# Performance work log

Hardware: AMD Instinct MI355X
Metric: run time of the kernel (lower is better)

Reference implementation:

```python
import jax, jax.numpy as jnp
import numpy as np

N_NODES = 100000
N_EDGES = 1000000
F_IN = 64
F_HID = 64
F_OUT = 2
NUM_GRAPHS = 64


def setup_inputs() -> dict:
    key = jax.random.key(0)
    ks = jax.random.split(key, 8)
    x = jax.random.normal(ks[0], (N_NODES, F_IN), dtype=jnp.float32)
    edge_index = jax.random.randint(ks[1], (2, N_EDGES), 0, N_NODES, dtype=jnp.int32)
    batch = jnp.sort(jax.random.randint(ks[2], (N_NODES,), 0, NUM_GRAPHS, dtype=jnp.int32))
    s1 = 1.0 / np.sqrt(F_IN)
    s2 = 1.0 / np.sqrt(F_HID)
    W1 = jax.random.normal(ks[3], (F_IN, F_HID), dtype=jnp.float32) * s1
    W2 = jax.random.normal(ks[4], (F_HID, F_HID), dtype=jnp.float32) * s2
    W3 = jax.random.normal(ks[5], (F_HID, F_HID), dtype=jnp.float32) * s2
    Wlin = jax.random.normal(ks[6], (F_HID, F_OUT), dtype=jnp.float32) * s2
    return {
        "x": x, "edge_index": edge_index, "batch": batch,
        "W1": W1, "b1": jnp.zeros((F_HID,), jnp.float32),
        "W2": W2, "b2": jnp.zeros((F_HID,), jnp.float32),
        "W3": W3, "b3": jnp.zeros((F_HID,), jnp.float32),
        "Wlin": Wlin, "blin": jnp.zeros((F_OUT,), jnp.float32),
    }


def _gcn_norm(edge_index, n_nodes):
    # add self-loops, compute symmetric D^-1/2 (A+I) D^-1/2 edge weights
    loops = jnp.arange(n_nodes, dtype=edge_index.dtype)
    src = jnp.concatenate([edge_index[0], loops])  # message source j
    dst = jnp.concatenate([edge_index[1], loops])  # aggregation target i
    deg = jax.ops.segment_sum(jnp.ones_like(dst, dtype=jnp.float32), dst,
                              num_segments=n_nodes)
    dinv = jnp.where(deg > 0, jax.lax.rsqrt(deg), 0.0)
    norm = dinv[src] * dinv[dst]  # [E+N]
    return src, dst, norm


def _gcn_conv(h, W, b, src, dst, norm, n_nodes):
    h = h @ W                                    # [N, F] dense transform first (PyG order)
    msg = h[src] * norm[:, None]                 # gather + scale  [E+N, F]
    agg = jax.ops.segment_sum(msg, dst, num_segments=n_nodes)
    return agg + b


def reference(x, edge_index, batch, W1, b1, W2, b2, W3, b3, Wlin, blin):
    n = x.shape[0]
    src, dst, norm = _gcn_norm(edge_index, n)
    h = jax.nn.relu(_gcn_conv(x, W1, b1, src, dst, norm, n))
    h = jax.nn.relu(_gcn_conv(h, W2, b2, src, dst, norm, n))
    h = _gcn_conv(h, W3, b3, src, dst, norm, n)
    # global mean pool over graphs
    sums = jax.ops.segment_sum(h, batch, num_segments=NUM_GRAPHS)        # [G, F]
    cnts = jax.ops.segment_sum(jnp.ones((n,), jnp.float32), batch,
                               num_segments=NUM_GRAPHS)
    pooled = sums / jnp.maximum(cnts, 1.0)[:, None]
    # dropout(p=0.1) is identity in eval mode
    return pooled @ Wlin + blin
```

## Files before the change

### kernel.cpp

```cpp
#include <hip/hip_runtime.h>

#define FDIM 64

typedef unsigned short u16;
typedef unsigned int u32;
typedef float v2f __attribute__((ext_vector_type(2)));

__device__ __forceinline__ u16 f2bf(float x) {
    unsigned int u = __float_as_uint(x);
    return (u16)((u + 0x7fff + ((u >> 16) & 1)) >> 16);
}
__device__ __forceinline__ float bf2f(u16 h) {
    return __uint_as_float(((unsigned int)h) << 16);
}
__device__ __forceinline__ u32 pk_fp8x4(float a, float b, float c, float d) {
    u32 p = __builtin_amdgcn_cvt_pk_fp8_f32(a, b, 0, false);
    p = __builtin_amdgcn_cvt_pk_fp8_f32(c, d, p, true);
    return p;
}


template <bool BF16IN>
__device__ __forceinline__ void mm_tile64(
    const void* __restrict__ ain, const float* __restrict__ bias, int do_relu,
    u32* __restrict__ t, int n, int blk,
    float (*__restrict__ As)[FDIM + 1], float* __restrict__ Ws)
{
    int tid = threadIdx.x;
    int r0 = blk * 64;

    #pragma unroll
    for (int i = 0; i < 4; ++i) {
        int idx = tid + 256 * i;
        int r = idx >> 4;
        int kq = idx & 15;
        float4 v = make_float4(0.f, 0.f, 0.f, 0.f);
        int R = r0 + r;
        if (R < n) {
            if (BF16IN) {
                ushort4 h = ((const ushort4*)ain)[(size_t)R * 16 + kq];
                v.x = bf2f(h.x); v.y = bf2f(h.y); v.z = bf2f(h.z); v.w = bf2f(h.w);
            } else {
                v = ((const float4*)ain)[(size_t)R * 16 + kq];
            }
            if (bias != nullptr) {
                float4 b = ((const float4*)bias)[kq];
                v.x += b.x; v.y += b.y; v.z += b.z; v.w += b.w;
            }
            if (do_relu) {
                v.x = fmaxf(v.x, 0.f); v.y = fmaxf(v.y, 0.f);
                v.z = fmaxf(v.z, 0.f); v.w = fmaxf(v.w, 0.f);
            }
        }
        As[r][kq * 4 + 0] = v.x;
        As[r][kq * 4 + 1] = v.y;
        As[r][kq * 4 + 2] = v.z;
        As[r][kq * 4 + 3] = v.w;
    }
    __syncthreads();

    int rq = tid >> 4;
    int cq = tid & 15;
    float acc[4][4];
    #pragma unroll
    for (int i = 0; i < 4; ++i)
        #pragma unroll
        for (int j = 0; j < 4; ++j) acc[i][j] = 0.f;

    const float4* Ws4 = (const float4*)Ws;
    #pragma unroll 4
    for (int k = 0; k < FDIM; ++k) {
        float4 w = Ws4[k * 16 + cq];
        float a[4];
        #pragma unroll
        for (int i = 0; i < 4; ++i) a[i] = As[rq * 4 + i][k];
        #pragma unroll
        for (int i = 0; i < 4; ++i) {
            acc[i][0] = fmaf(a[i], w.x, acc[i][0]);
            acc[i][1] = fmaf(a[i], w.y, acc[i][1]);
            acc[i][2] = fmaf(a[i], w.z, acc[i][2]);
            acc[i][3] = fmaf(a[i], w.w, acc[i][3]);
        }
    }

    #pragma unroll
    for (int i = 0; i < 4; ++i) {
        int R = r0 + rq * 4 + i;
        if (R < n)
            t[(size_t)R * 16 + cq] =
                pk_fp8x4(acc[i][0], acc[i][1], acc[i][2], acc[i][3]);
    }
}

__global__ __launch_bounds__(256) void k_matmul_h(
    const u16* __restrict__ ain, const float* __restrict__ Wm,
    const float* __restrict__ bias, u32* __restrict__ t, int n)
{
    __shared__ float As[64][FDIM + 1];
    __shared__ float Ws[FDIM * FDIM];
    int tid = threadIdx.x;
    #pragma unroll
    for (int i = 0; i < 4; ++i)
        ((float4*)Ws)[tid + 256 * i] = ((const float4*)Wm)[tid + 256 * i];
    mm_tile64<true>(ain, bias, 1, t, n, blockIdx.x, As, Ws);
}


__global__ __launch_bounds__(256) void k_mm_fill(
    const float* __restrict__ x, const float* __restrict__ W1,
    u32* __restrict__ t,
    const int* __restrict__ src, const int* __restrict__ dst,
    int* __restrict__ cnt, int* __restrict__ csr,
    int n, int E, int cap, int fill_blocks)
{
    __shared__ float As[64][FDIM + 1];
    __shared__ float Ws[FDIM * FDIM];

    if ((int)blockIdx.x < fill_blocks) {
        int stride = fill_blocks * 256;
        int e = blockIdx.x * 256 + threadIdx.x;
        for (; e + 7 * stride < E; e += 8 * stride) {
            int d[8], s[8], p[8];
            #pragma unroll
            for (int u = 0; u < 8; ++u)
                d[u] = __builtin_nontemporal_load(&dst[e + u * stride]);
            #pragma unroll
            for (int u = 0; u < 8; ++u)
                s[u] = __builtin_nontemporal_load(&src[e + u * stride]);
            #pragma unroll
            for (int u = 0; u < 8; ++u) p[u] = atomicAdd(&cnt[d[u]], 1);
            #pragma unroll
            for (int u = 0; u < 8; ++u)
                if (p[u] < cap) csr[(size_t)d[u] * cap + p[u]] = s[u];
        }
        for (; e < E; e += stride) {
            int d = dst[e];
            int p = atomicAdd(&cnt[d], 1);
            if (p < cap) csr[(size_t)d * cap + p] = src[e];
        }
        return;
    }

    int blk = blockIdx.x - fill_blocks;
    int tid = threadIdx.x;
    #pragma unroll
    for (int i = 0; i < 4; ++i)
        ((float4*)Ws)[tid + 256 * i] = ((const float4*)W1)[tid + 256 * i];
    mm_tile64<false>(x, nullptr, 0, t, n, blk, As, Ws);
}


__device__ __forceinline__ float4 agg_node(
    int i, const int* __restrict__ cnt, const int* __restrict__ csr,
    const u32* __restrict__ t, int cap, int li, int nbase)
{
    int deg = cnt[i];
    float di = rsqrtf((float)deg + 1.0f);
    int m = deg < cap ? deg : cap;

    u32 sp = t[(size_t)i * 16 + li];
    v2f s0 = __builtin_amdgcn_cvt_pk_f32_fp8(sp, false);
    v2f s1 = __builtin_amdgcn_cvt_pk_f32_fp8(sp, true);
    float4 A0 = make_float4(s0.x * di, s0.y * di, s1.x * di, s1.y * di);
    float4 A1 = make_float4(0.f, 0.f, 0.f, 0.f);
    float4 A2 = make_float4(0.f, 0.f, 0.f, 0.f);
    float4 A3 = make_float4(0.f, 0.f, 0.f, 0.f);

    const int* row = csr + (size_t)i * cap;

    for (int c0 = 0; c0 < m; c0 += 16) {
        int cm = m - c0; if (cm > 16) cm = 16;
        int sv = 0; float dvv = 0.f;
        if (li < cm) {
            sv = __builtin_nontemporal_load(&row[c0 + li]);
            dvv = rsqrtf((float)cnt[sv] + 1.0f);
        }
        int jv[16]; float dj[16]; u32 v[16];
        #pragma unroll
        for (int u = 0; u < 16; ++u) {
            jv[u] = __shfl(sv, nbase + u);
            dj[u] = __shfl(dvv, nbase + u);
        }
        #pragma unroll
        for (int u = 0; u < 16; ++u) v[u] = t[(size_t)jv[u] * 16 + li];
        #pragma unroll
        for (int u = 0; u < 16; ++u) {
            v2f x0 = __builtin_amdgcn_cvt_pk_f32_fp8(v[u], false);
            v2f x1 = __builtin_amdgcn_cvt_pk_f32_fp8(v[u], true);
            float4* Ap = (u & 3) == 0 ? &A0 : (u & 3) == 1 ? &A1 :
                         (u & 3) == 2 ? &A2 : &A3;
            Ap->x = fmaf(x0.x, dj[u], Ap->x);
            Ap->y = fmaf(x0.y, dj[u], Ap->y);
            Ap->z = fmaf(x1.x, dj[u], Ap->z);
            Ap->w = fmaf(x1.y, dj[u], Ap->w);
        }
    }

    float4 O;
    O.x = ((A0.x + A1.x) + (A2.x + A3.x)) * di;
    O.y = ((A0.y + A1.y) + (A2.y + A3.y)) * di;
    O.z = ((A0.z + A1.z) + (A2.z + A3.z)) * di;
    O.w = ((A0.w + A1.w) + (A2.w + A3.w)) * di;
    return O;
}


__global__ __launch_bounds__(256) void k_aggregate(
    const int* __restrict__ cnt, const int* __restrict__ csr,
    const u32* __restrict__ t, uint2* __restrict__ aggh, int n, int cap)
{
    int tid = threadIdx.x;
    long long gw = ((long long)blockIdx.x * 256 + tid) >> 6;
    int lane = tid & 63;
    int sub = lane >> 4;
    int li  = lane & 15;
    long long il = gw * 4 + sub;
    if (il >= n) return;
    int i = (int)il;

    float4 O = agg_node(i, cnt, csr, t, cap, li, sub << 4);
    uint2 pk;
    pk.x = ((u32)f2bf(O.x)) | (((u32)f2bf(O.y)) << 16);
    pk.y = ((u32)f2bf(O.z)) | (((u32)f2bf(O.w)) << 16);
    aggh[(size_t)i * 16 + li] = pk;
}


__global__ __launch_bounds__(256) void k_agg_pool(
    const int* __restrict__ cnt, const int* __restrict__ csr,
    const u32* __restrict__ t, const int* __restrict__ batch,
    float* __restrict__ partial, int n, int cap, int npart)
{
    int g = blockIdx.x / npart;
    int part = blockIdx.x - g * npart;
    int tid = threadIdx.x;

    int lo = 0, hi = n;
    while (lo < hi) { int mid = (lo + hi) >> 1; if (batch[mid] < g) lo = mid + 1; else hi = mid; }
    int start = lo;
    hi = n;
    while (lo < hi) { int mid = (lo + hi) >> 1; if (batch[mid] <= g) lo = mid + 1; else hi = mid; }
    int end = lo;

    int group = tid >> 4;
    int li = tid & 15;
    int lane = tid & 63;
    int nbase = (lane >> 4) << 4;

    float4 acc = make_float4(0.f, 0.f, 0.f, 0.f);
    for (int i = start + part * 16 + group; i < end; i += npart * 16) {
        float4 O = agg_node(i, cnt, csr, t, cap, li, nbase);
        acc.x += O.x; acc.y += O.y; acc.z += O.z; acc.w += O.w;
    }

    __shared__ float4 red[16][16];
    red[group][li] = acc;
    __syncthreads();
    if (tid < 16) {
        float4 s = make_float4(0.f, 0.f, 0.f, 0.f);
        #pragma unroll
        for (int q = 0; q < 16; ++q) {
            s.x += red[q][tid].x; s.y += red[q][tid].y;
            s.z += red[q][tid].z; s.w += red[q][tid].w;
        }
        ((float4*)partial)[((size_t)g * npart + part) * 16 + tid] = s;
    }
}

__global__ __launch_bounds__(64) void k_pool2(
    const float* __restrict__ partial, const int* __restrict__ batch,
    const float* __restrict__ b3, const float* __restrict__ Wlin,
    const float* __restrict__ blin, float* __restrict__ out,
    int n, int fout, int npart)
{
    int g = blockIdx.x;
    int tid = threadIdx.x;

    int lo = 0, hi = n;
    while (lo < hi) { int mid = (lo + hi) >> 1; if (batch[mid] < g) lo = mid + 1; else hi = mid; }
    int start = lo;
    hi = n;
    while (lo < hi) { int mid = (lo + hi) >> 1; if (batch[mid] <= g) lo = mid + 1; else hi = mid; }
    int cnt = lo - start;

    __shared__ float pooled[64];
    float v = 0.f;
    for (int p = 0; p < npart; ++p)
        v += partial[((size_t)g * npart + p) * 64 + tid];
    pooled[tid] = (cnt > 0) ? (v / (float)cnt + b3[tid]) : 0.f;
    __syncthreads();
    if (tid < fout) {
        float o = blin[tid];
        for (int k = 0; k < 64; ++k) o += pooled[k] * Wlin[k * fout + tid];
        out[(size_t)g * fout + tid] = o;
    }
}


extern "C" void kernel_launch(void* const* d_in, const int* in_sizes, int n_in,
                              void* d_out, int out_size, void* d_ws, size_t ws_size,
                              hipStream_t stream) {
    const float* x     = (const float*)d_in[0];
    const int*   ei    = (const int*)d_in[1];
    const int*   batch = (const int*)d_in[2];
    const float* W1 = (const float*)d_in[3];
    const float* b1 = (const float*)d_in[4];
    const float* W2 = (const float*)d_in[5];
    const float* b2 = (const float*)d_in[6];
    const float* W3 = (const float*)d_in[7];
    const float* b3 = (const float*)d_in[8];
    const float* Wl = (const float*)d_in[9];
    const float* bl = (const float*)d_in[10];

    int n = in_sizes[0] / 64;
    int E = in_sizes[1] / 2;
    int fout = in_sizes[10];
    int ngraphs = out_size / fout;

    const int* srcp = ei;
    const int* dstp = ei + E;

    const int npart = 16;

    float* ws   = (float*)d_ws;
    u32*   agg  = (u32*)ws;
    u32*   t    = agg + (size_t)n * 32;
    float* partial = (float*)(t + (size_t)n * 16);
    int* cnt    = (int*)(partial + 64 * npart * 64);
    int* csr    = cnt + n;

    size_t fixed = (size_t)n * 32 * 4 + (size_t)n * 16 * 4 +
                   64 * npart * 64 * 4 + (size_t)n * 4;
    int cap = 64;
    while (cap > 32 && fixed + (size_t)n * cap * 4 > ws_size) cap -= 8;

    int nb_ag = (int)((((long long)(n + 3) / 4) * 64 + 255) / 256);
    int mm_blocks = (n + 63) / 64;
    int fill_blocks = 256;

    hipMemsetAsync(cnt, 0, (size_t)n * sizeof(int), stream);
    k_mm_fill<<<fill_blocks + mm_blocks, 256, 0, stream>>>(
        x, W1, t, srcp, dstp, cnt, csr, n, E, cap, fill_blocks);

    k_aggregate<<<nb_ag, 256, 0, stream>>>(cnt, csr, t, (uint2*)agg, n, cap);
    k_matmul_h<<<mm_blocks, 256, 0, stream>>>((const u16*)agg, W2, b1, t, n);
    k_aggregate<<<nb_ag, 256, 0, stream>>>(cnt, csr, t, (uint2*)agg, n, cap);
    k_matmul_h<<<mm_blocks, 256, 0, stream>>>((const u16*)agg, W3, b2, t, n);
    k_agg_pool<<<ngraphs * npart, 256, 0, stream>>>(cnt, csr, t, batch,
                                                    partial, n, cap, npart);
    k_pool2<<<ngraphs, 64, 0, stream>>>(partial, batch, b3, Wl, bl,
                                        (float*)d_out, n, fout, npart);
}
```

Baseline: 270.5 us.

## Prescale transformed features by source degree norm to drop per-edge rsqrt

Layers 2 and 3 now fold the source-side D^-1/2 factor into the matmul epilogue before fp8 packing. The aggregation can then sum neighbor features without gathering each neighbor's degree or computing an rsqrt per edge. Padding lanes point at a zeroed dummy row at index n, so no per-lane weight is needed. The trade-off is a small extra cnt read in the matmul, and a change in fp8 quantization because features are scaled before packing, which may affect accuracy.

```diff
diff --git a/kernel.cpp b/kernel.cpp
--- a/kernel.cpp
+++ b/kernel.cpp
@@ -23,6 +23,7 @@
 template <bool BF16IN>
 __device__ __forceinline__ void mm_tile64(
     const void* __restrict__ ain, const float* __restrict__ bias, int do_relu,
+    const int* __restrict__ scale_cnt,
     u32* __restrict__ t, int n, int blk,
     float (*__restrict__ As)[FDIM + 1], float* __restrict__ Ws)
 {
@@ -86,15 +87,21 @@
     #pragma unroll
     for (int i = 0; i < 4; ++i) {
         int R = r0 + rq * 4 + i;
-        if (R < n)
+        if (R < n) {
+            float sc = 1.0f;
+            if (scale_cnt != nullptr)
+                sc = rsqrtf((float)scale_cnt[R] + 1.0f);
             t[(size_t)R * 16 + cq] =
-                pk_fp8x4(acc[i][0], acc[i][1], acc[i][2], acc[i][3]);
+                pk_fp8x4(acc[i][0] * sc, acc[i][1] * sc,
+                         acc[i][2] * sc, acc[i][3] * sc);
+        }
     }
 }
 
 __global__ __launch_bounds__(256) void k_matmul_h(
     const u16* __restrict__ ain, const float* __restrict__ Wm,
-    const float* __restrict__ bias, u32* __restrict__ t, int n)
+    const float* __restrict__ bias, const int* __restrict__ cnt,
+    u32* __restrict__ t, int n)
 {
     __shared__ float As[64][FDIM + 1];
     __shared__ float Ws[FDIM * FDIM];
@@ -102,7 +109,7 @@
     #pragma unroll
     for (int i = 0; i < 4; ++i)
         ((float4*)Ws)[tid + 256 * i] = ((const float4*)Wm)[tid + 256 * i];
-    mm_tile64<true>(ain, bias, 1, t, n, blockIdx.x, As, Ws);
+    mm_tile64<true>(ain, bias, 1, cnt, t, n, blockIdx.x, As, Ws);
 }
 
 
@@ -146,13 +153,14 @@
     #pragma unroll
     for (int i = 0; i < 4; ++i)
         ((float4*)Ws)[tid + 256 * i] = ((const float4*)W1)[tid + 256 * i];
-    mm_tile64<false>(x, nullptr, 0, t, n, blk, As, Ws);
-}
-
-
+    mm_tile64<false>(x, nullptr, 0, nullptr, t, n, blk, As, Ws);
+}
+
+
+template <bool SCALED>
 __device__ __forceinline__ float4 agg_node(
     int i, const int* __restrict__ cnt, const int* __restrict__ csr,
-    const u32* __restrict__ t, int cap, int li, int nbase)
+    const u32* __restrict__ t, int cap, int li, int nbase, int zr)
 {
     int deg = cnt[i];
     float di = rsqrtf((float)deg + 1.0f);
@@ -161,7 +169,8 @@
     u32 sp = t[(size_t)i * 16 + li];
     v2f s0 = __builtin_amdgcn_cvt_pk_f32_fp8(sp, false);
     v2f s1 = __builtin_amdgcn_cvt_pk_f32_fp8(sp, true);
-    float4 A0 = make_float4(s0.x * di, s0.y * di, s1.x * di, s1.y * di);
+    float sm = SCALED ? 1.0f : di;
+    float4 A0 = make_float4(s0.x * sm, s0.y * sm, s1.x * sm, s1.y * sm);
     float4 A1 = make_float4(0.f, 0.f, 0.f, 0.f);
     float4 A2 = make_float4(0.f, 0.f, 0.f, 0.f);
     float4 A3 = make_float4(0.f, 0.f, 0.f, 0.f);
@@ -170,29 +179,45 @@
 
     for (int c0 = 0; c0 < m; c0 += 16) {
         int cm = m - c0; if (cm > 16) cm = 16;
-        int sv = 0; float dvv = 0.f;
+        int sv = zr; float dvv = 0.f;
         if (li < cm) {
             sv = __builtin_nontemporal_load(&row[c0 + li]);
-            dvv = rsqrtf((float)cnt[sv] + 1.0f);
-        }
-        int jv[16]; float dj[16]; u32 v[16];
-        #pragma unroll
-        for (int u = 0; u < 16; ++u) {
-            jv[u] = __shfl(sv, nbase + u);
-            dj[u] = __shfl(dvv, nbase + u);
-        }
-        #pragma unroll
-        for (int u = 0; u < 16; ++u) v[u] = t[(size_t)jv[u] * 16 + li];
-        #pragma unroll
-        for (int u = 0; u < 16; ++u) {
-            v2f x0 = __builtin_amdgcn_cvt_pk_f32_fp8(v[u], false);
-            v2f x1 = __builtin_amdgcn_cvt_pk_f32_fp8(v[u], true);
-            float4* Ap = (u & 3) == 0 ? &A0 : (u & 3) == 1 ? &A1 :
-                         (u & 3) == 2 ? &A2 : &A3;
-            Ap->x = fmaf(x0.x, dj[u], Ap->x);
-            Ap->y = fmaf(x0.y, dj[u], Ap->y);
-            Ap->z = fmaf(x1.x, dj[u], Ap->z);
-            Ap->w = fmaf(x1.y, dj[u], Ap->w);
+            if (!SCALED) dvv = rsqrtf((float)cnt[sv] + 1.0f);
+        }
+        if (SCALED) {
+            int jv[16]; u32 v[16];
+            #pragma unroll
+            for (int u = 0; u < 16; ++u) jv[u] = __shfl(sv, nbase + u);
+            #pragma unroll
+            for (int u = 0; u < 16; ++u) v[u] = t[(size_t)jv[u] * 16 + li];
+            #pragma unroll
+            for (int u = 0; u < 16; ++u) {
+                v2f x0 = __builtin_amdgcn_cvt_pk_f32_fp8(v[u], false);
+                v2f x1 = __builtin_amdgcn_cvt_pk_f32_fp8(v[u], true);
+                float4* Ap = (u & 3) == 0 ? &A0 : (u & 3) == 1 ? &A1 :
+                             (u & 3) == 2 ? &A2 : &A3;
+                Ap->x += x0.x; Ap->y += x0.y; Ap->z += x1.x; Ap->w += x1.y;
+            }
+        } else {
+            int jv[16]; float dj[16]; u32 v[16];
+            #pragma unroll
+            for (int u = 0; u < 16; ++u) {
+                jv[u] = __shfl(sv, nbase + u);
+                dj[u] = __shfl(dvv, nbase + u);
+            }
+            #pragma unroll
+            for (int u = 0; u < 16; ++u) v[u] = t[(size_t)jv[u] * 16 + li];
+            #pragma unroll
+            for (int u = 0; u < 16; ++u) {
+                v2f x0 = __builtin_amdgcn_cvt_pk_f32_fp8(v[u], false);
+                v2f x1 = __builtin_amdgcn_cvt_pk_f32_fp8(v[u], true);
+                float4* Ap = (u & 3) == 0 ? &A0 : (u & 3) == 1 ? &A1 :
+                             (u & 3) == 2 ? &A2 : &A3;
+                Ap->x = fmaf(x0.x, dj[u], Ap->x);
+                Ap->y = fmaf(x0.y, dj[u], Ap->y);
+                Ap->z = fmaf(x1.x, dj[u], Ap->z);
+                Ap->w = fmaf(x1.y, dj[u], Ap->w);
+            }
         }
     }
 
@@ -205,6 +230,7 @@
 }
 
 
+template <bool SCALED>
 __global__ __launch_bounds__(256) void k_aggregate(
     const int* __restrict__ cnt, const int* __restrict__ csr,
     const u32* __restrict__ t, uint2* __restrict__ aggh, int n, int cap)
@@ -218,7 +244,7 @@
     if (il >= n) return;
     int i = (int)il;
 
-    float4 O = agg_node(i, cnt, csr, t, cap, li, sub << 4);
+    float4 O = agg_node<SCALED>(i, cnt, csr, t, cap, li, sub << 4, n);
     uint2 pk;
     pk.x = ((u32)f2bf(O.x)) | (((u32)f2bf(O.y)) << 16);
     pk.y = ((u32)f2bf(O.z)) | (((u32)f2bf(O.w)) << 16);
@@ -249,7 +275,7 @@
 
     float4 acc = make_float4(0.f, 0.f, 0.f, 0.f);
     for (int i = start + part * 16 + group; i < end; i += npart * 16) {
-        float4 O = agg_node(i, cnt, csr, t, cap, li, nbase);
+        float4 O = agg_node<true>(i, cnt, csr, t, cap, li, nbase, n);
         acc.x += O.x; acc.y += O.y; acc.z += O.z; acc.w += O.w;
     }
 
@@ -325,11 +351,11 @@
     float* ws   = (float*)d_ws;
     u32*   agg  = (u32*)ws;
     u32*   t    = agg + (size_t)n * 32;
-    float* partial = (float*)(t + (size_t)n * 16);
+    float* partial = (float*)(t + (size_t)(n + 1) * 16);
     int* cnt    = (int*)(partial + 64 * npart * 64);
     int* csr    = cnt + n;
 
-    size_t fixed = (size_t)n * 32 * 4 + (size_t)n * 16 * 4 +
+    size_t fixed = (size_t)n * 32 * 4 + (size_t)(n + 1) * 16 * 4 +
                    64 * npart * 64 * 4 + (size_t)n * 4;
     int cap = 64;
     while (cap > 32 && fixed + (size_t)n * cap * 4 > ws_size) cap -= 8;
@@ -339,13 +365,14 @@
     int fill_blocks = 256;
 
     hipMemsetAsync(cnt, 0, (size_t)n * sizeof(int), stream);
+    hipMemsetAsync(t + (size_t)n * 16, 0, 64, stream);
     k_mm_fill<<<fill_blocks + mm_blocks, 256, 0, stream>>>(
         x, W1, t, srcp, dstp, cnt, csr, n, E, cap, fill_blocks);
 
-    k_aggregate<<<nb_ag, 256, 0, stream>>>(cnt, csr, t, (uint2*)agg, n, cap);
-    k_matmul_h<<<mm_blocks, 256, 0, stream>>>((const u16*)agg, W2, b1, t, n);
-    k_aggregate<<<nb_ag, 256, 0, stream>>>(cnt, csr, t, (uint2*)agg, n, cap);
-    k_matmul_h<<<mm_blocks, 256, 0, stream>>>((const u16*)agg, W3, b2, t, n);
+    k_aggregate<false><<<nb_ag, 256, 0, stream>>>(cnt, csr, t, (uint2*)agg, n, cap);
+    k_matmul_h<<<mm_blocks, 256, 0, stream>>>((const u16*)agg, W2, b1, cnt, t, n);
+    k_aggregate<true><<<nb_ag, 256, 0, stream>>>(cnt, csr, t, (uint2*)agg, n, cap);
+    k_matmul_h<<<mm_blocks, 256, 0, stream>>>((const u16*)agg, W3, b2, cnt, t, n);
     k_agg_pool<<<ngraphs * npart, 256, 0, stream>>>(cnt, csr, t, batch,
                                                     partial, n, cap, npart);
     k_pool2<<<ngraphs, 64, 0, stream>>>(partial, batch, b3, Wl, bl,
```

After: 272.4 us. Within noise of the previous version (+0.7%).
